# Kernel tuning notes

Measured on AMD Instinct MI355X. Metric: run time of the kernel, lower is better.

Reference implementation:

```python
import jax, jax.numpy as jnp
import numpy as np
from jax.ops import segment_sum

N_NODES = 100000
N_EDGES = 1600000
HIDDEN = 128


def gcn_conv(x, src, dst, w, W, b, num_nodes):
    """PyG GCNConv: add self-loops (weight 1), symmetric deg^-1/2 normalization,
    gather from src, scatter-add to dst. x: [N, Fin], W: [Fin, Fout]."""
    loop = jnp.arange(num_nodes, dtype=src.dtype)
    s = jnp.concatenate([src, loop])
    d = jnp.concatenate([dst, loop])
    ww = jnp.concatenate([w, jnp.ones((num_nodes,), dtype=w.dtype)])
    deg = segment_sum(ww, d, num_segments=num_nodes)           # [N]
    dis = jnp.where(deg > 0, jax.lax.rsqrt(jnp.where(deg > 0, deg, 1.0)), 0.0)
    norm = dis[s] * ww * dis[d]                                # [E+N]
    h = x @ W                                                  # [N, Fout]
    msg = norm[:, None] * h[s]                                 # [E+N, Fout]
    out = segment_sum(msg, d, num_segments=num_nodes)          # [N, Fout]
    return out + b


def setup_inputs() -> dict:
    key = jax.random.key(0)
    ks = jax.random.split(key, 12)
    h = HIDDEN
    sc = lambda fan_in: 1.0 / np.sqrt(fan_in)
    return {
        "x": jax.random.normal(ks[0], (N_NODES, 1), dtype=jnp.float32),
        "edge_index": jax.random.randint(ks[1], (2, N_EDGES), 0, N_NODES, dtype=jnp.int64),
        "edge_weight": jax.random.uniform(ks[2], (N_EDGES,), dtype=jnp.float32),
        "W1": jax.random.normal(ks[3], (1, h), dtype=jnp.float32) * sc(1),
        "b1": jnp.zeros((h,), dtype=jnp.float32),
        "W2": jax.random.normal(ks[4], (h, 2 * h), dtype=jnp.float32) * sc(h),
        "b2": jnp.zeros((2 * h,), dtype=jnp.float32),
        "Wl1": jax.random.normal(ks[5], (2 * h, h), dtype=jnp.float32) * sc(2 * h),
        "bl1": jnp.zeros((h,), dtype=jnp.float32),
        "Wl2": jax.random.normal(ks[6], (h, 1), dtype=jnp.float32) * sc(h),
        "bl2": jnp.zeros((1,), dtype=jnp.float32),
    }


def reference(x, edge_index, edge_weight, W1, b1, W2, b2, Wl1, bl1, Wl2, bl2):
    n = x.shape[0]
    src, dst = edge_index[0], edge_index[1]
    h = jax.nn.relu(gcn_conv(x, src, dst, edge_weight, W1, b1, n))
    h = jax.nn.relu(gcn_conv(h, src, dst, edge_weight, W2, b2, n))
    h = jax.nn.relu(h @ Wl1 + bl1)
    return h @ Wl2 + bl2
```

## Files before the change

### kernel.cpp

```cpp
#include <hip/hip_runtime.h>


#define HD 128
#define HD2 256
#define BSHIFT 8
#define BNODES 256
#define SRCBITS 17

typedef __attribute__((ext_vector_type(8))) short bf8_t;
typedef __attribute__((ext_vector_type(4))) float f32x4;

static inline size_t align256(size_t x) { return (x + 255) & ~(size_t)255; }

__device__ inline ushort f2bf(float f) {
    uint u = __float_as_uint(f);
    uint r = u + 0x7fffu + ((u >> 16) & 1u);
    return (ushort)(r >> 16);
}
__device__ inline uint packbf(float a, float b) {
    return (uint)f2bf(a) | ((uint)f2bf(b) << 16);
}

__global__ __launch_bounds__(256) void k_part(const int* __restrict__ ei,
                                              const float* __restrict__ ew,
                                              int* __restrict__ bfill,
                                              uint2* __restrict__ stg,
                                              int E, int nbuck, int cap) {
    __shared__ int lcnt[4][512];
    __shared__ int lbase[4][512];
    int tid = threadIdx.x;
    int wvid = tid >> 6;
    for (int i = tid; i < nbuck; i += 256) {
        lcnt[0][i] = 0; lcnt[1][i] = 0; lcnt[2][i] = 0; lcnt[3][i] = 0;
    }
    __syncthreads();
    bool is64 = (ei[1] == 0) && (ei[3] == 0) && (ei[5] == 0) && (ei[7] == 0);
    int e0 = blockIdx.x * 2048;
    uint pack[8]; uint wb[8]; int bkt[8]; int rank[8];
    for (int u = 0; u < 8; u++) {
        int e = e0 + u * 256 + tid;
        bkt[u] = -1;
        if (e < E) {
            int s, d;
            if (is64) { s = ei[2 * e]; d = ei[2 * (E + e)]; }
            else      { s = ei[e];     d = ei[E + e]; }
            bkt[u] = d >> BSHIFT;
            pack[u] = ((uint)(d & (BNODES - 1)) << SRCBITS) | (uint)s;
            wb[u] = __float_as_uint(ew[e]);
            rank[u] = atomicAdd(&lcnt[wvid][bkt[u]], 1);
        }
    }
    __syncthreads();
    for (int i = tid; i < nbuck; i += 256) {
        int t0 = lcnt[0][i], t1 = lcnt[1][i], t2 = lcnt[2][i], t3 = lcnt[3][i];
        int tot = t0 + t1 + t2 + t3;
        int base = tot ? atomicAdd(&bfill[i], tot) : 0;
        lbase[0][i] = base;
        lbase[1][i] = base + t0;
        lbase[2][i] = base + t0 + t1;
        lbase[3][i] = base + t0 + t1 + t2;
    }
    __syncthreads();
    for (int u = 0; u < 8; u++)
        if (bkt[u] >= 0)
            stg[(size_t)bkt[u] * cap + lbase[wvid][bkt[u]] + rank[u]] =
                make_uint2(pack[u], wb[u]);
}

__global__ __launch_bounds__(512) void k_bscan(const int* __restrict__ bfill,
                                               int* __restrict__ cvbase,
                                               int* __restrict__ rowptr,
                                               int nbuck, int N, int E) {
    __shared__ int ws[8];
    int tid = threadIdx.x;
    int lane = tid & 63, wvid = tid >> 6;
    int a = (tid < nbuck) ? bfill[tid] : 0;
    int v = a;
    for (int off = 1; off < 64; off <<= 1) {
        int u = __shfl_up(v, off);
        if (lane >= off) v += u;
    }
    if (lane == 63) ws[wvid] = v;
    __syncthreads();
    int wpre = 0;
    for (int k = 0; k < wvid; k++) wpre += ws[k];
    if (tid < nbuck) cvbase[tid] = v + wpre - a;
    if (tid == 0) rowptr[N] = E;
}

__global__ __launch_bounds__(512) void k_fine(const uint2* __restrict__ stg,
                                              const int* __restrict__ bfill,
                                              const int* __restrict__ cvbase,
                                              const float* __restrict__ x,
                                              float* __restrict__ dis,
                                              float* __restrict__ p,
                                              int* __restrict__ rowptr,
                                              int2* __restrict__ cv,
                                              int cap, int N) {
    __shared__ int cnt_l[BNODES];
    __shared__ int base_l[BNODES];
    __shared__ float degf[BNODES];
    __shared__ int wsum[4];
    int b = blockIdx.x, tid = threadIdx.x;
    int n = bfill[b];
    int cb = cvbase[b];
    const uint2* s = stg + (size_t)b * cap;
    if (tid < BNODES) { cnt_l[tid] = 0; degf[tid] = 1.0f; }
    __syncthreads();
    for (int i = tid; i < n; i += 512)
        atomicAdd(&cnt_l[s[i].x >> SRCBITS], 1);
    __syncthreads();
    int lane = tid & 63, wvid = tid >> 6;
    int a = 0;
    if (tid < BNODES) { a = cnt_l[tid]; cnt_l[tid] = 0; }
    int v = a;
    for (int off = 1; off < 64; off <<= 1) {
        int u = __shfl_up(v, off);
        if (lane >= off) v += u;
    }
    if (wvid < 4 && lane == 63) wsum[wvid] = v;
    __syncthreads();
    if (tid < BNODES) {
        int wpre = 0;
        for (int k = 0; k < wvid; k++) wpre += wsum[k];
        base_l[tid] = v + wpre - a;
    }
    __syncthreads();
    for (int i = tid; i < n; i += 512) {
        uint2 r = s[i];
        int dl = r.x >> SRCBITS;
        int src = (int)(r.x & ((1u << SRCBITS) - 1));
        int pos = cb + base_l[dl] + atomicAdd(&cnt_l[dl], 1);
        cv[pos] = make_int2(src, (int)r.y);
        atomicAdd(&degf[dl], __uint_as_float(r.y));
    }
    __syncthreads();
    int gid = (b << BSHIFT) + tid;
    if (tid < BNODES && gid < N) {
        rowptr[gid] = cb + base_l[tid];
        float r = rsqrtf(degf[tid]);
        dis[gid] = r;
        p[gid] = r * x[gid];
    }
}

__global__ void k_prepB(const float* __restrict__ W2, const float* __restrict__ Wl1,
                        ushort* __restrict__ Bt1, ushort* __restrict__ Bt2) {
    int o = blockIdx.x * blockDim.x + threadIdx.x;
    if (o >= 32768) return;
    {
        int k0 = o & 7, n = (o >> 3) & 255, k8 = o >> 11;
        Bt1[o] = f2bf(W2[(size_t)(k8 * 8 + k0) * 256 + n]);
    }
    {
        int k0 = o & 7, n = (o >> 3) & 127, k8 = o >> 10;
        Bt2[o] = f2bf(Wl1[(size_t)(k8 * 8 + k0) * 128 + n]);
    }
}

__global__ __launch_bounds__(256) void k_q(const int* __restrict__ rowptr,
                                           const int2* __restrict__ cv,
                                           const float* __restrict__ dis,
                                           const float* __restrict__ p,
                                           float2* __restrict__ tp, int N) {
    int gid = blockIdx.x * blockDim.x + threadIdx.x;
    int wid = gid >> 4;
    int sl = threadIdx.x & 15;
    if (wid >= N) return;
    int beg = rowptr[wid], end = rowptr[wid + 1];
    float s = 0.0f;
    for (int i = beg + sl; i < end; i += 16) {
        int2 pr = cv[i];
        s += __int_as_float(pr.y) * p[pr.x];
    }
    s += __shfl_xor(s, 1);
    s += __shfl_xor(s, 2);
    s += __shfl_xor(s, 4);
    s += __shfl_xor(s, 8);
    if (sl == 0) {
        float r = dis[wid];
        tp[wid] = make_float2(r * (s + p[wid]), r);
    }
}

__global__ __launch_bounds__(256) void k_agg(const int* __restrict__ rowptr,
                                             const int2* __restrict__ cv,
                                             const float2* __restrict__ tp,
                                             const float* __restrict__ W1,
                                             const float* __restrict__ b1,
                                             uint* __restrict__ z, int N) {
    __shared__ float4 eb[4][32];
    int tid = threadIdx.x;
    int wvid = tid >> 6, lane = tid & 63;
    int wid = (blockIdx.x * blockDim.x + tid) >> 6;
    if (wid >= N) return;
    float2 w1 = *(const float2*)(W1 + lane * 2);
    float2 bb = *(const float2*)(b1 + lane * 2);
    int beg = rowptr[wid], end = rowptr[wid + 1];
    float ax0 = 0.0f, ay0 = 0.0f, ax1 = 0.0f, ay1 = 0.0f;
    for (int base = beg; base < end; base += 64) {
        int eidx = base + lane;
        float wd = 0.0f, tt = 0.0f;
        if (eidx < end) {
            int2 pr = cv[eidx];
            float2 tps = tp[pr.x];
            wd = __int_as_float(pr.y) * tps.y;
            tt = tps.x;
        }
        ((float2*)&eb[wvid][0])[lane] = make_float2(wd, tt);
        int m = min(64, end - base);
        const float4* ebp = &eb[wvid][0];
        int halves = (m + 1) >> 1;
        int u = 0;
        for (; u + 2 <= halves; u += 2) {
            float4 e2 = ebp[u];
            float4 e3 = ebp[u + 1];
            ax0 = fmaf(e2.x, fmaxf(fmaf(e2.y, w1.x, bb.x), 0.0f), ax0);
            ay0 = fmaf(e2.x, fmaxf(fmaf(e2.y, w1.y, bb.y), 0.0f), ay0);
            ax1 = fmaf(e2.z, fmaxf(fmaf(e2.w, w1.x, bb.x), 0.0f), ax1);
            ay1 = fmaf(e2.z, fmaxf(fmaf(e2.w, w1.y, bb.y), 0.0f), ay1);
            ax0 = fmaf(e3.x, fmaxf(fmaf(e3.y, w1.x, bb.x), 0.0f), ax0);
            ay0 = fmaf(e3.x, fmaxf(fmaf(e3.y, w1.y, bb.y), 0.0f), ay0);
            ax1 = fmaf(e3.z, fmaxf(fmaf(e3.w, w1.x, bb.x), 0.0f), ax1);
            ay1 = fmaf(e3.z, fmaxf(fmaf(e3.w, w1.y, bb.y), 0.0f), ay1);
        }
        if (u < halves) {
            float4 e2 = ebp[u];
            ax0 = fmaf(e2.x, fmaxf(fmaf(e2.y, w1.x, bb.x), 0.0f), ax0);
            ay0 = fmaf(e2.x, fmaxf(fmaf(e2.y, w1.y, bb.y), 0.0f), ay0);
            ax1 = fmaf(e2.z, fmaxf(fmaf(e2.w, w1.x, bb.x), 0.0f), ax1);
            ay1 = fmaf(e2.z, fmaxf(fmaf(e2.w, w1.y, bb.y), 0.0f), ay1);
        }
    }
    float ax = ax0 + ax1, ay = ay0 + ay1;
    float2 tpd = tp[wid];
    float rd = tpd.y;
    float s0 = rd * fmaxf(fmaf(tpd.x, w1.x, bb.x), 0.0f);
    float s1 = rd * fmaxf(fmaf(tpd.x, w1.y, bb.y), 0.0f);
    z[(size_t)wid * 64 + lane] = packbf(rd * (ax + s0), rd * (ay + s1));
}

__global__ __launch_bounds__(256) void k_mlp(const ushort* __restrict__ A,
                                             const ushort* __restrict__ Bt1,
                                             const ushort* __restrict__ Bt2,
                                             const float* __restrict__ b2,
                                             const float* __restrict__ bl1,
                                             const float* __restrict__ wl2,
                                             const float* __restrict__ bl2,
                                             float* __restrict__ out, int M) {
    __shared__ ushort sB1[4096];
    __shared__ ushort sB2[4096];
    __shared__ ushort st[4][32][40];
    int tid = threadIdx.x;
    int wv = tid >> 6, lane = tid & 63;
    int l15 = lane & 15, quad = lane >> 4;
    int row0 = blockIdx.x * 128 + wv * 32;
    int r0 = row0 + l15;      r0 = r0 < M ? r0 : M - 1;
    int r1 = row0 + 16 + l15; r1 = r1 < M ? r1 : M - 1;

    bf8_t a1[2][4];
    for (int kc = 0; kc < 4; kc++) {
        a1[0][kc] = *(const bf8_t*)(A + (size_t)r0 * 128 + kc * 32 + quad * 8);
        a1[1][kc] = *(const bf8_t*)(A + (size_t)r1 * 128 + kc * 32 + quad * 8);
    }
    f32x4 acc2[2][8];
    for (int i = 0; i < 2; i++)
        for (int j = 0; j < 8; j++) acc2[i][j] = (f32x4){0.f, 0.f, 0.f, 0.f};

    for (int c = 0; c < 8; c++) {
        {
            uint4* s1 = (uint4*)sB1;
            for (int i = tid; i < 512; i += 256) {
                int r = i >> 5, j = i & 31;
                s1[i] = ((const uint4*)(Bt1 + ((size_t)(r * 256 + c * 32)) * 8))[j];
            }
            uint4* s2 = (uint4*)sB2;
            const uint4* g2 = (const uint4*)(Bt2 + (size_t)c * 4096);
            for (int i = tid; i < 512; i += 256) s2[i] = g2[i];
        }
        __syncthreads();
        f32x4 acc1[2][2];
        for (int i = 0; i < 2; i++)
            for (int j = 0; j < 2; j++) acc1[i][j] = (f32x4){0.f, 0.f, 0.f, 0.f};
        for (int kc = 0; kc < 4; kc++)
            for (int nt = 0; nt < 2; nt++) {
                bf8_t b = *(const bf8_t*)(sB1 +
                    ((size_t)((kc * 4 + quad) * 32 + nt * 16 + l15)) * 8);
                acc1[0][nt] = __builtin_amdgcn_mfma_f32_16x16x32_bf16(a1[0][kc], b, acc1[0][nt], 0, 0, 0);
                acc1[1][nt] = __builtin_amdgcn_mfma_f32_16x16x32_bf16(a1[1][kc], b, acc1[1][nt], 0, 0, 0);
            }
        for (int nt = 0; nt < 2; nt++) {
            float bbv = b2[c * 32 + nt * 16 + l15];
            for (int mt = 0; mt < 2; mt++)
                for (int rg = 0; rg < 4; rg++)
                    st[wv][mt * 16 + quad * 4 + rg][nt * 16 + l15] =
                        f2bf(fmaxf(acc1[mt][nt][rg] + bbv, 0.f));
        }
        bf8_t a2_0 = *(const bf8_t*)&st[wv][l15][quad * 8];
        bf8_t a2_1 = *(const bf8_t*)&st[wv][16 + l15][quad * 8];
        for (int nt2 = 0; nt2 < 8; nt2++) {
            bf8_t b = *(const bf8_t*)(sB2 +
                ((size_t)(quad * 128 + nt2 * 16 + l15)) * 8);
            acc2[0][nt2] = __builtin_amdgcn_mfma_f32_16x16x32_bf16(a2_0, b, acc2[0][nt2], 0, 0, 0);
            acc2[1][nt2] = __builtin_amdgcn_mfma_f32_16x16x32_bf16(a2_1, b, acc2[1][nt2], 0, 0, 0);
        }
        __syncthreads();
    }
    float rs[2][4] = {};
    for (int nt2 = 0; nt2 < 8; nt2++) {
        int col = nt2 * 16 + l15;
        float bbv = bl1[col], ww = wl2[col];
        for (int mt = 0; mt < 2; mt++)
            for (int rg = 0; rg < 4; rg++)
                rs[mt][rg] += fmaxf(acc2[mt][nt2][rg] + bbv, 0.f) * ww;
    }
    float base = bl2[0];
    for (int mt = 0; mt < 2; mt++)
        for (int rg = 0; rg < 4; rg++) {
            float s = rs[mt][rg];
            s += __shfl_xor(s, 1);
            s += __shfl_xor(s, 2);
            s += __shfl_xor(s, 4);
            s += __shfl_xor(s, 8);
            int row = row0 + mt * 16 + quad * 4 + rg;
            if (l15 == 0 && row < M) out[row] = s + base;
        }
}

extern "C" void kernel_launch(void* const* d_in, const int* in_sizes, int n_in,
                              void* d_out, int out_size, void* d_ws, size_t ws_size,
                              hipStream_t stream) {
    const float* x   = (const float*)d_in[0];
    const int*   ei  = (const int*)d_in[1];
    const float* ew  = (const float*)d_in[2];
    const float* W1  = (const float*)d_in[3];
    const float* b1  = (const float*)d_in[4];
    const float* W2  = (const float*)d_in[5];
    const float* b2  = (const float*)d_in[6];
    const float* Wl1 = (const float*)d_in[7];
    const float* bl1 = (const float*)d_in[8];
    const float* Wl2 = (const float*)d_in[9];
    const float* bl2 = (const float*)d_in[10];
    float* out = (float*)d_out;
    const int N = in_sizes[0];
    const int E = in_sizes[2];

    const int nbuck = (N + BNODES - 1) >> BSHIFT;
    const int cap = ((E / nbuck) * 5) / 4 + 1024;

    char* w = (char*)d_ws;
    size_t off = 0;
    auto alloc = [&](size_t bytes) -> void* {
        void* p = w + off;
        off = align256(off + bytes);
        return p;
    };
    uint*   z      = (uint*)alloc((size_t)N * 64 * 4);
    float2* tp     = (float2*)alloc((size_t)N * 8);
    float*  dis    = (float*)alloc((size_t)N * 4);
    float*  p_     = (float*)alloc((size_t)N * 4);
    int*    rowptr = (int*)alloc((size_t)(N + 1) * 4);
    int2*   cv     = (int2*)alloc((size_t)E * 8);
    uint2*  stg    = (uint2*)alloc((size_t)nbuck * cap * 8);
    int*    bfill  = (int*)alloc(512 * 4);
    int*    cvbase = (int*)alloc(512 * 4);
    ushort* Bt1    = (ushort*)alloc(32768 * 2);
    ushort* Bt2    = (ushort*)alloc(32768 * 2);

    hipMemsetAsync(bfill, 0, 512 * 4, stream);
    k_part<<<(E + 2047) / 2048, 256, 0, stream>>>(ei, ew, bfill, stg, E, nbuck, cap);
    k_bscan<<<1, 512, 0, stream>>>(bfill, cvbase, rowptr, nbuck, N, E);
    k_fine<<<nbuck, 512, 0, stream>>>(stg, bfill, cvbase, x, dis, p_, rowptr, cv, cap, N);
    k_prepB<<<128, 256, 0, stream>>>(W2, Wl1, Bt1, Bt2);
    k_q<<<(N * 16 + 255) / 256, 256, 0, stream>>>(rowptr, cv, dis, p_, tp, N);
    k_agg<<<(N + 3) / 4, 256, 0, stream>>>(rowptr, cv, tp, W1, b1, z, N);
    k_mlp<<<(N + 127) / 128, 256, 0, stream>>>((const ushort*)z, Bt1, Bt2,
                                               b2, bl1, Wl2, bl2, out, N);
}
```

Baseline: 219.9 us.

## Fold bucket scan into k_fine, merge init kernels, drop LDS staging in MLP

The memset and the weight bf16 conversion are merged into one init kernel. The single-block bucket scan kernel is removed, and each k_fine block now computes its own prefix by reducing bfill over the preceding buckets. Together these cut three launches and their serialization gaps. k_mlp no longer stages the B matrices through shared memory with barriers and instead reads B fragments straight from global/L2, which removes __syncthreads but adds global-load latency inside the MFMA loop.

```diff
diff --git a/kernel.cpp b/kernel.cpp
--- a/kernel.cpp
+++ b/kernel.cpp
@@ -19,6 +19,22 @@
 }
 __device__ inline uint packbf(float a, float b) {
     return (uint)f2bf(a) | ((uint)f2bf(b) << 16);
+}
+
+__global__ void k_init(const float* __restrict__ W2, const float* __restrict__ Wl1,
+                       ushort* __restrict__ Bt1, ushort* __restrict__ Bt2,
+                       int* __restrict__ bfill) {
+    int o = blockIdx.x * blockDim.x + threadIdx.x;
+    if (o < 512) bfill[o] = 0;
+    if (o >= 32768) return;
+    {
+        int k0 = o & 7, n = (o >> 3) & 255, k8 = o >> 11;
+        Bt1[o] = f2bf(W2[(size_t)(k8 * 8 + k0) * 256 + n]);
+    }
+    {
+        int k0 = o & 7, n = (o >> 3) & 127, k8 = o >> 10;
+        Bt2[o] = f2bf(Wl1[(size_t)(k8 * 8 + k0) * 128 + n]);
+    }
 }
 
 __global__ __launch_bounds__(256) void k_part(const int* __restrict__ ei,
@@ -67,53 +83,37 @@
                 make_uint2(pack[u], wb[u]);
 }
 
-__global__ __launch_bounds__(512) void k_bscan(const int* __restrict__ bfill,
-                                               int* __restrict__ cvbase,
-                                               int* __restrict__ rowptr,
-                                               int nbuck, int N, int E) {
-    __shared__ int ws[8];
-    int tid = threadIdx.x;
-    int lane = tid & 63, wvid = tid >> 6;
-    int a = (tid < nbuck) ? bfill[tid] : 0;
-    int v = a;
-    for (int off = 1; off < 64; off <<= 1) {
-        int u = __shfl_up(v, off);
-        if (lane >= off) v += u;
-    }
-    if (lane == 63) ws[wvid] = v;
-    __syncthreads();
-    int wpre = 0;
-    for (int k = 0; k < wvid; k++) wpre += ws[k];
-    if (tid < nbuck) cvbase[tid] = v + wpre - a;
-    if (tid == 0) rowptr[N] = E;
-}
-
 __global__ __launch_bounds__(512) void k_fine(const uint2* __restrict__ stg,
                                               const int* __restrict__ bfill,
-                                              const int* __restrict__ cvbase,
                                               const float* __restrict__ x,
                                               float* __restrict__ dis,
                                               float* __restrict__ p,
                                               int* __restrict__ rowptr,
                                               int2* __restrict__ cv,
-                                              int cap, int N) {
+                                              int cap, int N, int E, int nbuck) {
     __shared__ int cnt_l[BNODES];
     __shared__ int base_l[BNODES];
     __shared__ float degf[BNODES];
-    __shared__ int wsum[4];
+    __shared__ int wsum[8];
     int b = blockIdx.x, tid = threadIdx.x;
+    int lane = tid & 63, wvid = tid >> 6;
+    int a = (tid < b && tid < nbuck) ? bfill[tid] : 0;
+    for (int off = 32; off > 0; off >>= 1) a += __shfl_xor(a, off);
+    if (lane == 0) wsum[wvid] = a;
+    __syncthreads();
+    int cb = wsum[0] + wsum[1] + wsum[2] + wsum[3] +
+             wsum[4] + wsum[5] + wsum[6] + wsum[7];
     int n = bfill[b];
-    int cb = cvbase[b];
+    if (b == nbuck - 1 && tid == 0) rowptr[N] = E;
     const uint2* s = stg + (size_t)b * cap;
     if (tid < BNODES) { cnt_l[tid] = 0; degf[tid] = 1.0f; }
     __syncthreads();
     for (int i = tid; i < n; i += 512)
         atomicAdd(&cnt_l[s[i].x >> SRCBITS], 1);
     __syncthreads();
-    int lane = tid & 63, wvid = tid >> 6;
-    int a = 0;
-    if (tid < BNODES) { a = cnt_l[tid]; cnt_l[tid] = 0; }
-    int v = a;
+    int c = 0;
+    if (tid < BNODES) { c = cnt_l[tid]; cnt_l[tid] = 0; }
+    int v = c;
     for (int off = 1; off < 64; off <<= 1) {
         int u = __shfl_up(v, off);
         if (lane >= off) v += u;
@@ -123,7 +123,7 @@
     if (tid < BNODES) {
         int wpre = 0;
         for (int k = 0; k < wvid; k++) wpre += wsum[k];
-        base_l[tid] = v + wpre - a;
+        base_l[tid] = v + wpre - c;
     }
     __syncthreads();
     for (int i = tid; i < n; i += 512) {
@@ -141,20 +141,6 @@
         float r = rsqrtf(degf[tid]);
         dis[gid] = r;
         p[gid] = r * x[gid];
-    }
-}
-
-__global__ void k_prepB(const float* __restrict__ W2, const float* __restrict__ Wl1,
-                        ushort* __restrict__ Bt1, ushort* __restrict__ Bt2) {
-    int o = blockIdx.x * blockDim.x + threadIdx.x;
-    if (o >= 32768) return;
-    {
-        int k0 = o & 7, n = (o >> 3) & 255, k8 = o >> 11;
-        Bt1[o] = f2bf(W2[(size_t)(k8 * 8 + k0) * 256 + n]);
-    }
-    {
-        int k0 = o & 7, n = (o >> 3) & 127, k8 = o >> 10;
-        Bt2[o] = f2bf(Wl1[(size_t)(k8 * 8 + k0) * 128 + n]);
     }
 }
 
@@ -248,8 +234,6 @@
                                              const float* __restrict__ wl2,
                                              const float* __restrict__ bl2,
                                              float* __restrict__ out, int M) {
-    __shared__ ushort sB1[4096];
-    __shared__ ushort sB2[4096];
     __shared__ ushort st[4][32][40];
     int tid = threadIdx.x;
     int wv = tid >> 6, lane = tid & 63;
@@ -268,51 +252,39 @@
         for (int j = 0; j < 8; j++) acc2[i][j] = (f32x4){0.f, 0.f, 0.f, 0.f};
 
     for (int c = 0; c < 8; c++) {
-        {
-            uint4* s1 = (uint4*)sB1;
-            for (int i = tid; i < 512; i += 256) {
-                int r = i >> 5, j = i & 31;
-                s1[i] = ((const uint4*)(Bt1 + ((size_t)(r * 256 + c * 32)) * 8))[j];
-            }
-            uint4* s2 = (uint4*)sB2;
-            const uint4* g2 = (const uint4*)(Bt2 + (size_t)c * 4096);
-            for (int i = tid; i < 512; i += 256) s2[i] = g2[i];
-        }
-        __syncthreads();
         f32x4 acc1[2][2];
         for (int i = 0; i < 2; i++)
             for (int j = 0; j < 2; j++) acc1[i][j] = (f32x4){0.f, 0.f, 0.f, 0.f};
         for (int kc = 0; kc < 4; kc++)
             for (int nt = 0; nt < 2; nt++) {
-                bf8_t b = *(const bf8_t*)(sB1 +
-                    ((size_t)((kc * 4 + quad) * 32 + nt * 16 + l15)) * 8);
+                bf8_t b = *(const bf8_t*)(Bt1 +
+                    ((size_t)(kc * 4 + quad) * 256 + c * 32 + nt * 16 + l15) * 8);
                 acc1[0][nt] = __builtin_amdgcn_mfma_f32_16x16x32_bf16(a1[0][kc], b, acc1[0][nt], 0, 0, 0);
                 acc1[1][nt] = __builtin_amdgcn_mfma_f32_16x16x32_bf16(a1[1][kc], b, acc1[1][nt], 0, 0, 0);
             }
         for (int nt = 0; nt < 2; nt++) {
-            float bbv = b2[c * 32 + nt * 16 + l15];
+            float bb = b2[c * 32 + nt * 16 + l15];
             for (int mt = 0; mt < 2; mt++)
                 for (int rg = 0; rg < 4; rg++)
                     st[wv][mt * 16 + quad * 4 + rg][nt * 16 + l15] =
-                        f2bf(fmaxf(acc1[mt][nt][rg] + bbv, 0.f));
+                        f2bf(fmaxf(acc1[mt][nt][rg] + bb, 0.f));
         }
         bf8_t a2_0 = *(const bf8_t*)&st[wv][l15][quad * 8];
         bf8_t a2_1 = *(const bf8_t*)&st[wv][16 + l15][quad * 8];
         for (int nt2 = 0; nt2 < 8; nt2++) {
-            bf8_t b = *(const bf8_t*)(sB2 +
-                ((size_t)(quad * 128 + nt2 * 16 + l15)) * 8);
+            bf8_t b = *(const bf8_t*)(Bt2 +
+                ((size_t)(c * 4 + quad) * 128 + nt2 * 16 + l15) * 8);
             acc2[0][nt2] = __builtin_amdgcn_mfma_f32_16x16x32_bf16(a2_0, b, acc2[0][nt2], 0, 0, 0);
             acc2[1][nt2] = __builtin_amdgcn_mfma_f32_16x16x32_bf16(a2_1, b, acc2[1][nt2], 0, 0, 0);
         }
-        __syncthreads();
     }
     float rs[2][4] = {};
     for (int nt2 = 0; nt2 < 8; nt2++) {
         int col = nt2 * 16 + l15;
-        float bbv = bl1[col], ww = wl2[col];
+        float bb = bl1[col], ww = wl2[col];
         for (int mt = 0; mt < 2; mt++)
             for (int rg = 0; rg < 4; rg++)
-                rs[mt][rg] += fmaxf(acc2[mt][nt2][rg] + bbv, 0.f) * ww;
+                rs[mt][rg] += fmaxf(acc2[mt][nt2][rg] + bb, 0.f) * ww;
     }
     float base = bl2[0];
     for (int mt = 0; mt < 2; mt++)
@@ -363,15 +335,12 @@
     int2*   cv     = (int2*)alloc((size_t)E * 8);
     uint2*  stg    = (uint2*)alloc((size_t)nbuck * cap * 8);
     int*    bfill  = (int*)alloc(512 * 4);
-    int*    cvbase = (int*)alloc(512 * 4);
     ushort* Bt1    = (ushort*)alloc(32768 * 2);
     ushort* Bt2    = (ushort*)alloc(32768 * 2);
 
-    hipMemsetAsync(bfill, 0, 512 * 4, stream);
+    k_init<<<128, 256, 0, stream>>>(W2, Wl1, Bt1, Bt2, bfill);
     k_part<<<(E + 2047) / 2048, 256, 0, stream>>>(ei, ew, bfill, stg, E, nbuck, cap);
-    k_bscan<<<1, 512, 0, stream>>>(bfill, cvbase, rowptr, nbuck, N, E);
-    k_fine<<<nbuck, 512, 0, stream>>>(stg, bfill, cvbase, x, dis, p_, rowptr, cv, cap, N);
-    k_prepB<<<128, 256, 0, stream>>>(W2, Wl1, Bt1, Bt2);
+    k_fine<<<nbuck, 512, 0, stream>>>(stg, bfill, x, dis, p_, rowptr, cv, cap, N, E, nbuck);
     k_q<<<(N * 16 + 255) / 256, 256, 0, stream>>>(rowptr, cv, dis, p_, tp, N);
     k_agg<<<(N + 3) / 4, 256, 0, stream>>>(rowptr, cv, tp, W1, b1, z, N);
     k_mlp<<<(N + 127) / 128, 256, 0, stream>>>((const ushort*)z, Bt1, Bt2,
```

New measurement: 211.6 us. 1.04x faster.
